# Performance work log

Measured on AMD Instinct MI355X. Metric: run time of the kernel, lower is better.

Reference implementation:

```python
import jax, jax.numpy as jnp
import numpy as np

# 4D convolution via lax.conv_general_dilated with 4 spatial dims.
# Layout: input (N, C, D, H, W, T), kernel (O, I, d, h, w, t).
DN = ('NCDHWT', 'OIDHWT', 'NCDHWT')


def conv4d(x, w, b, pad):
    # torch Conv2d/Conv4d is cross-correlation, matching lax.conv_general_dilated
    y = jax.lax.conv_general_dilated(
        x, w, window_strides=(1, 1, 1, 1),
        padding=[(pad, pad)] * 4, dimension_numbers=DN)
    return y + b.reshape(1, -1, 1, 1, 1, 1)


def _kaiming(key, shape):
    fan_out = shape[0] * int(np.prod(shape[2:]))
    std = np.sqrt(2.0 / fan_out)
    return (jax.random.normal(key, shape, dtype=jnp.float32) * std).astype(jnp.float32)


def setup_inputs() -> dict:
    key = jax.random.key(0)
    ks = jax.random.split(key, 11)
    B, W, H = 256, 16, 16
    corr = jax.random.normal(ks[0], (B, W * H, W, H), dtype=jnp.float32)
    w1 = _kaiming(ks[1], (1, 1, 17, 17, 9, 9))
    w2 = _kaiming(ks[2], (1, 1, 7, 7, 7, 7))
    w3 = _kaiming(ks[3], (1, 1, 5, 5, 5, 5))
    w4 = _kaiming(ks[4], (1, 1, 3, 3, 3, 3))
    w5 = _kaiming(ks[5], (1, 1, 8, 8, 1, 1))
    b1 = jax.random.normal(ks[6], (1,), dtype=jnp.float32) * 0.01
    b2 = jax.random.normal(ks[7], (1,), dtype=jnp.float32) * 0.01
    b3 = jax.random.normal(ks[8], (1,), dtype=jnp.float32) * 0.01
    b4 = jax.random.normal(ks[9], (1,), dtype=jnp.float32) * 0.01
    b5 = jax.random.normal(ks[10], (1,), dtype=jnp.float32) * 0.01
    return {"corr": corr, "w1": w1, "b1": b1, "w2": w2, "b2": b2,
            "w3": w3, "b3": b3, "w4": w4, "b4": b4, "w5": w5, "b5": b5}


def reference(corr, w1, b1, w2, b2, w3, b3, w4, b4, w5, b5):
    B, HW, W, H = corr.shape
    x = corr.reshape(B, 1, W, H, W, H)          # (B,1,16,16,16,16)
    x = jax.nn.relu(conv4d(x, w1, b1, 4))       # (B,1, 8, 8,16,16)
    x = jax.nn.relu(conv4d(x, w2, b2, 3))
    x = jax.nn.relu(conv4d(x, w3, b3, 2))
    x = jax.nn.relu(conv4d(x, w4, b4, 1))
    out = jax.nn.sigmoid(conv4d(x, w5, b5, 0))  # (B,1, 1, 1,16,16)
    return out.reshape(B, 1, W, H)
```

## Files before the change

kernel.cpp:

```cpp
#include <hip/hip_runtime.h>
#include <math.h>


typedef short bf16x8 __attribute__((ext_vector_type(8)));
typedef float f32x4 __attribute__((ext_vector_type(4)));
typedef unsigned int u32x4 __attribute__((ext_vector_type(4)));

#define XTS 64
#define NROWS 396
#define ZROW 384

__device__ __forceinline__ int xts(int row, int col) {
  return row * XTS + (col ^ ((row & 7) << 3));
}

__device__ __forceinline__ unsigned short f2bf(float f) {
  unsigned int u = __float_as_uint(f);
  u += 0x7fffu + ((u >> 16) & 1u);
  return (unsigned short)(u >> 16);
}

template <int KSZ, int PAD>
__device__ __forceinline__ void build_mid(const float* __restrict__ w,
                                          unsigned short* __restrict__ Bg, int gid) {
  const int lane = gid & 63;
  const int n_tile = (gid >> 6) & 3;
  const int chunk = (gid >> 8) & 1;
  const int tap = gid >> 9;
  const int kw = tap / KSZ, kt = tap - kw * KSZ;
  const int dh_o = n_tile * 16 + (lane & 15);
  const int d_o = dh_o >> 3, h_o = dh_o & 7;
  const int kbase = chunk * 32 + (lane >> 4) * 8;
  unsigned int pk[4];
#pragma unroll
  for (int p = 0; p < 4; ++p) {
    unsigned short half[2];
#pragma unroll
    for (int s = 0; s < 2; ++s) {
      const int k = kbase + p * 2 + s;
      const int d_i = k >> 3, h_i = k & 7;
      const int kd = d_i - d_o + PAD, kh = h_i - h_o + PAD;
      float v = 0.f;
      if (kd >= 0 && kd < KSZ && kh >= 0 && kh < KSZ)
        v = w[((kd * KSZ + kh) * KSZ + kw) * KSZ + kt];
      half[s] = f2bf(v);
    }
    pk[p] = (unsigned int)half[0] | ((unsigned int)half[1] << 16);
  }
  *(int4*)(Bg + (size_t)gid * 8) = make_int4(pk[0], pk[1], pk[2], pk[3]);
}

__global__ __launch_bounds__(256) void build_all(const float* __restrict__ w1,
                                                 const float* __restrict__ w2,
                                                 const float* __restrict__ w3,
                                                 const float* __restrict__ w4,
                                                 unsigned short* __restrict__ Bg1,
                                                 unsigned short* __restrict__ Bg2,
                                                 unsigned short* __restrict__ Bg3,
                                                 unsigned short* __restrict__ Bg4) {
  const int bid = blockIdx.x, tid = threadIdx.x;
  if (bid < 648) {
    const int gid = bid * 256 + tid;
    const int lane = gid & 63;
    const int n_tile = (gid >> 6) & 3;
    const int chunk = (gid >> 8) & 7;
    const int kwkt = gid >> 11;
    const int kw = kwkt / 9, kt = kwkt - kw * 9;
    const int dh_o = n_tile * 16 + (lane & 15);
    const int d_o = dh_o >> 3, h_o = dh_o & 7;
    const int kbase = chunk * 32 + (lane >> 4) * 8;
    unsigned int pk[4];
#pragma unroll
    for (int p = 0; p < 4; ++p) {
      unsigned short half[2];
#pragma unroll
      for (int s = 0; s < 2; ++s) {
        const int k = kbase + p * 2 + s;
        const int d_i = k >> 4, h_i = k & 15;
        const int kd = d_i - d_o + 4, kh = h_i - h_o + 4;
        float v = 0.f;
        if (kd >= 0 && kd < 17 && kh >= 0 && kh < 17)
          v = w1[((kd * 17 + kh) * 9 + kw) * 9 + kt];
        half[s] = f2bf(v);
      }
      pk[p] = (unsigned int)half[0] | ((unsigned int)half[1] << 16);
    }
    *(int4*)(Bg1 + (size_t)gid * 8) = make_int4(pk[0], pk[1], pk[2], pk[3]);
  } else if (bid < 746) {
    build_mid<7, 3>(w2, Bg2, (bid - 648) * 256 + tid);
  } else if (bid < 796) {
    build_mid<5, 2>(w3, Bg3, (bid - 746) * 256 + tid);
  } else {
    build_mid<3, 1>(w4, Bg4, (bid - 796) * 256 + tid);
  }
}

__device__ __forceinline__ void l1_load(const unsigned short* XT,
                                        const unsigned short* __restrict__ Bt,
                                        const int (&ar)[4], int kt, int col0, int col1,
                                        bf16x8 (&A)[8], bf16x8 (&B)[8]) {
#pragma unroll
  for (int m = 0; m < 4; ++m) {
    const int row = ar[m] + kt;
    const int sw = (row & 7) << 3;
    A[m] = *(const bf16x8*)&XT[row * XTS + (col0 ^ sw)];
    A[4 + m] = *(const bf16x8*)&XT[row * XTS + (col1 ^ sw)];
  }
#pragma unroll
  for (int c = 0; c < 2; ++c)
#pragma unroll
    for (int n = 0; n < 4; ++n)
      B[c * 4 + n] = *(const bf16x8*)(Bt + (size_t)kt * 16384 + c * 2048 + n * 512);
}

__device__ __forceinline__ void mfma16(const bf16x8 (&A)[8], const bf16x8 (&B)[8],
                                       f32x4 (&acc)[4][4]) {
#pragma unroll
  for (int c = 0; c < 2; ++c)
#pragma unroll
    for (int m = 0; m < 4; ++m)
#pragma unroll
      for (int n = 0; n < 4; ++n)
        acc[m][n] = __builtin_amdgcn_mfma_f32_16x16x32_bf16(A[c * 4 + m], B[c * 4 + n],
                                                            acc[m][n], 0, 0, 0);
}

__global__ __launch_bounds__(256) void conv_l1_mfma(const float* __restrict__ x,
                                                    const unsigned short* __restrict__ Bg,
                                                    float* __restrict__ P) {
  __shared__ __align__(16) unsigned short XT[NROWS * XTS];
  const int bx = blockIdx.x;
  const int b = bx >> 2, q = bx & 3;
  const int tid = threadIdx.x;
  const int lane = tid & 63, wave = tid >> 6;
  const int quad = lane >> 4, tl = lane & 15;
  const float* xb = x + (size_t)b * 65536;
  f32x4 acc[4][4] = {};

  for (int j = tid; j < (NROWS * XTS) / 8; j += 256)
    *(int4*)&XT[j * 8] = make_int4(0, 0, 0, 0);
  __syncthreads();

#pragma unroll
  for (int it = 0; it < 8; ++it) {
    const int i = tid + it * 256;
    const int dhp = i >> 6, wtq = i & 63;
    const int r0 = (wtq >> 2) * 24 + (wtq & 3) * 4 + 4;
    const float4 ra = *(const float4*)(xb + (size_t)(q * 64 + 2 * dhp) * 256 + wtq * 4);
    const float4 rb = *(const float4*)(xb + (size_t)(q * 64 + 2 * dhp + 1) * 256 + wtq * 4);
    const float a0[4] = {ra.x, ra.y, ra.z, ra.w};
    const float a1[4] = {rb.x, rb.y, rb.z, rb.w};
#pragma unroll
    for (int j = 0; j < 4; ++j) {
      const unsigned int p = (unsigned int)f2bf(a0[j]) | ((unsigned int)f2bf(a1[j]) << 16);
      *(unsigned int*)&XT[xts(r0 + j, dhp * 2)] = p;
    }
  }
  __syncthreads();

  const int chbase = q * 2;
  const unsigned short* Bt = Bg + (size_t)chbase * 2048 + lane * 8;
  const int col0 = quad * 8, col1 = col0 + 32;
  for (int kw = 0; kw < 9; ++kw) {
    int ar[4];
#pragma unroll
    for (int m = 0; m < 4; ++m) {
      const int w_i = wave * 4 + m + kw - 4;
      ar[m] = ((unsigned)w_i < 16u) ? (w_i * 24 + tl) : ZROW;
    }
    bf16x8 A0[8], B0[8], A1[8], B1[8];
    l1_load(XT, Bt, ar, 0, col0, col1, A0, B0);
#pragma unroll
    for (int kt = 0; kt < 9; ++kt) {
      if ((kt & 1) == 0) {
        if (kt < 8) l1_load(XT, Bt, ar, kt + 1, col0, col1, A1, B1);
        mfma16(A0, B0, acc);
      } else {
        if (kt < 8) l1_load(XT, Bt, ar, kt + 1, col0, col1, A0, B0);
        mfma16(A1, B1, acc);
      }
    }
    Bt += 9 * 16384;
  }

  float* Pb = P + (size_t)(q * 256 + b) * 16384;
#pragma unroll
  for (int m = 0; m < 4; ++m)
#pragma unroll
    for (int n = 0; n < 4; ++n) {
      const int dh_o = n * 16 + tl;
      const int wt0 = wave * 64 + m * 16 + quad * 4;
      *(float4*)&Pb[(size_t)dh_o * 256 + wt0] = *(const float4*)&acc[m][n];
    }
}

__device__ __forceinline__ void tl_load(const unsigned short* XT,
                                        const unsigned short* __restrict__ Bt,
                                        const int (&ar)[2], int kt, int nh, int col0,
                                        int col1, bf16x8 (&A)[4], bf16x8 (&B)[4]) {
#pragma unroll
  for (int m = 0; m < 2; ++m) {
    const int row = ar[m] + kt;
    const int sw = (row & 7) << 3;
    A[m] = *(const bf16x8*)&XT[row * XTS + (col0 ^ sw)];
    A[2 + m] = *(const bf16x8*)&XT[row * XTS + (col1 ^ sw)];
  }
#pragma unroll
  for (int c = 0; c < 2; ++c)
#pragma unroll
    for (int n = 0; n < 2; ++n)
      B[c * 2 + n] =
          *(const bf16x8*)(Bt + (size_t)kt * 4096 + c * 2048 + (nh * 2 + n) * 512);
}

__device__ __forceinline__ void mfma8(const bf16x8 (&A)[4], const bf16x8 (&B)[4],
                                      f32x4 (&acc)[2][2]) {
#pragma unroll
  for (int c = 0; c < 2; ++c)
#pragma unroll
    for (int m = 0; m < 2; ++m)
#pragma unroll
      for (int n = 0; n < 2; ++n)
        acc[m][n] = __builtin_amdgcn_mfma_f32_16x16x32_bf16(A[c * 2 + m], B[c * 2 + n],
                                                            acc[m][n], 0, 0, 0);
}

template <int KSZ, int PAD>
__device__ __forceinline__ void run_layer(unsigned short* XT,
                                          const unsigned short* __restrict__ Bg,
                                          const float bias, int mw, int nh, int lane,
                                          int quad, int tl) {
  f32x4 acc[2][2] = {};
  const unsigned short* Bt = Bg + lane * 8;
  const int col0 = quad * 8, col1 = col0 + 32;
  for (int kw = 0; kw < KSZ; ++kw) {
    int ar[2];
#pragma unroll
    for (int m = 0; m < 2; ++m) {
      const int w_i = mw * 2 + m + kw - PAD;
      ar[m] = ((unsigned)w_i < 16u) ? (w_i * 24 + tl + (4 - PAD)) : ZROW;
    }
    bf16x8 A0[4], B0[4], A1[4], B1[4];
    tl_load(XT, Bt, ar, 0, nh, col0, col1, A0, B0);
#pragma unroll
    for (int kt = 0; kt < KSZ; ++kt) {
      if ((kt & 1) == 0) {
        if (kt < KSZ - 1) tl_load(XT, Bt, ar, kt + 1, nh, col0, col1, A1, B1);
        mfma8(A0, B0, acc);
      } else {
        if (kt < KSZ - 1) tl_load(XT, Bt, ar, kt + 1, nh, col0, col1, A0, B0);
        mfma8(A1, B1, acc);
      }
    }
    Bt += (size_t)KSZ * 4096;
  }
  __syncthreads();
#pragma unroll
  for (int m = 0; m < 2; ++m) {
    const int rbase = (mw * 2 + m) * 24 + quad * 4 + 4;
#pragma unroll
    for (int n = 0; n < 2; ++n) {
      const int col = (nh * 2 + n) * 16 + tl;
#pragma unroll
      for (int j = 0; j < 4; ++j)
        XT[xts(rbase + j, col)] = f2bf(fmaxf(acc[m][n][j] + bias, 0.f));
    }
  }
  __syncthreads();
}

__global__ __launch_bounds__(1024) void tail_fused(const float* __restrict__ P,
                                                   const unsigned short* __restrict__ Bg2,
                                                   const unsigned short* __restrict__ Bg3,
                                                   const unsigned short* __restrict__ Bg4,
                                                   const float* __restrict__ b1,
                                                   const float* __restrict__ b2,
                                                   const float* __restrict__ b3,
                                                   const float* __restrict__ b4,
                                                   const float* __restrict__ w5,
                                                   const float* __restrict__ b5,
                                                   float* __restrict__ out) {
  __shared__ __align__(16) unsigned short XT[NROWS * XTS];
  const int b = blockIdx.x;
  const int tid = threadIdx.x;
  const int lane = tid & 63, wave = tid >> 6;
  const int quad = lane >> 4, tl = lane & 15;
  const int mw = wave >> 1, nh = wave & 1;
  const float* p0 = P + (size_t)b * 16384;
  const float* p1 = p0 + (size_t)256 * 16384;
  const float* p2 = p0 + (size_t)512 * 16384;
  const float* p3 = p0 + (size_t)768 * 16384;
  const float bias1 = b1[0];

  for (int j = tid; j < (NROWS * XTS) / 8; j += 1024)
    *(int4*)&XT[j * 8] = make_int4(0, 0, 0, 0);
  __syncthreads();

#pragma unroll
  for (int it = 0; it < 2; ++it) {
    const int i = tid + it * 1024;
    const int dhp = i >> 6, wtq = i & 63;
    const int r0 = (wtq >> 2) * 24 + (wtq & 3) * 4 + 4;
    const size_t off0 = (size_t)(2 * dhp) * 256 + wtq * 4;
    const float4 r0a = *(const float4*)(p0 + off0);
    const float4 r0b = *(const float4*)(p1 + off0);
    const float4 r0c = *(const float4*)(p2 + off0);
    const float4 r0d = *(const float4*)(p3 + off0);
    const float4 r1a = *(const float4*)(p0 + off0 + 256);
    const float4 r1b = *(const float4*)(p1 + off0 + 256);
    const float4 r1c = *(const float4*)(p2 + off0 + 256);
    const float4 r1d = *(const float4*)(p3 + off0 + 256);
    float a0[4] = {r0a.x + r0b.x + r0c.x + r0d.x, r0a.y + r0b.y + r0c.y + r0d.y,
                   r0a.z + r0b.z + r0c.z + r0d.z, r0a.w + r0b.w + r0c.w + r0d.w};
    float a1[4] = {r1a.x + r1b.x + r1c.x + r1d.x, r1a.y + r1b.y + r1c.y + r1d.y,
                   r1a.z + r1b.z + r1c.z + r1d.z, r1a.w + r1b.w + r1c.w + r1d.w};
#pragma unroll
    for (int j = 0; j < 4; ++j) {
      const unsigned short lo = f2bf(fmaxf(a0[j] + bias1, 0.f));
      const unsigned short hi = f2bf(fmaxf(a1[j] + bias1, 0.f));
      const unsigned int p = (unsigned int)lo | ((unsigned int)hi << 16);
      *(unsigned int*)&XT[xts(r0 + j, dhp * 2)] = p;
    }
  }
  __syncthreads();

  run_layer<7, 3>(XT, Bg2, b2[0], mw, nh, lane, quad, tl);
  run_layer<5, 2>(XT, Bg3, b3[0], mw, nh, lane, quad, tl);
  run_layer<3, 1>(XT, Bg4, b4[0], mw, nh, lane, quad, tl);

  if (tid < 256) {
    const int wt = tid;
    const int r = (wt >> 4) * 24 + (wt & 15) + 4;
    float s = b5[0];
#pragma unroll
    for (int k8 = 0; k8 < 8; ++k8) {
      const u32x4 v = *(const u32x4*)&XT[xts(r, k8 * 8)];
      const unsigned int uu[4] = {(unsigned int)v.x, (unsigned int)v.y, (unsigned int)v.z,
                                  (unsigned int)v.w};
#pragma unroll
      for (int p = 0; p < 4; ++p) {
        const float lo = __uint_as_float(uu[p] << 16);
        const float hi = __uint_as_float(uu[p] & 0xFFFF0000u);
        s += lo * w5[k8 * 8 + p * 2] + hi * w5[k8 * 8 + p * 2 + 1];
      }
    }
    out[(size_t)b * 256 + wt] = 1.f / (1.f + expf(-s));
  }
}

extern "C" void kernel_launch(void* const* d_in, const int* in_sizes, int n_in,
                              void* d_out, int out_size, void* d_ws, size_t ws_size,
                              hipStream_t stream) {
  const float* corr = (const float*)d_in[0];
  const float* w1 = (const float*)d_in[1];
  const float* b1 = (const float*)d_in[2];
  const float* w2 = (const float*)d_in[3];
  const float* b2 = (const float*)d_in[4];
  const float* w3 = (const float*)d_in[5];
  const float* b3 = (const float*)d_in[6];
  const float* w4 = (const float*)d_in[7];
  const float* b4 = (const float*)d_in[8];
  const float* w5 = (const float*)d_in[9];
  const float* b5 = (const float*)d_in[10];

  float* P = (float*)d_ws;
  unsigned short* Bg1 = (unsigned short*)((char*)d_ws + (64u << 20));
  unsigned short* Bg2 = Bg1 + (size_t)81 * 8 * 4 * 64 * 8;
  unsigned short* Bg3 = Bg2 + (size_t)49 * 2 * 4 * 64 * 8;
  unsigned short* Bg4 = Bg3 + (size_t)25 * 2 * 4 * 64 * 8;

  build_all<<<814, 256, 0, stream>>>(w1, w2, w3, w4, Bg1, Bg2, Bg3, Bg4);
  conv_l1_mfma<<<1024, 256, 0, stream>>>(corr, Bg1, P);
  tail_fused<<<256, 1024, 0, stream>>>(P, Bg2, Bg3, Bg4, b1, b2, b3, b4, w5, b5,
                                       (float*)d_out);
}
```

Before: 303.2 us.

## Restructure tail layers with padded LDS layout, larger per-wave tiles, fewer threads

The fused tail kernel now runs 512 threads instead of 1024, and each wave computes a 4x2 grid of MFMA tiles instead of 2x2, so each A fragment is reused across more outputs. The LDS activation buffer moves from an XOR-swizzled layout with halo rows to a padded-stride (72) layout with a single shared zero row. Out-of-range taps in both w and t are redirected to that zero row, which removes the full-buffer zeroing pass. The per-tap loop is flattened across kw/kt with double-buffered loads. The layer-1 MFMA loop also gets s_setprio raised around its MFMA bursts. The risks are fewer resident waves to hide LDS latency and higher register pressure from the larger accumulators.

```diff
diff --git a/kernel.cpp b/kernel.cpp
--- a/kernel.cpp
+++ b/kernel.cpp
@@ -9,6 +9,7 @@
 #define XTS 64
 #define NROWS 396
 #define ZROW 384
+#define TTS 72
 
 __device__ __forceinline__ int xts(int row, int col) {
   return row * XTS + (col ^ ((row & 7) << 3));
@@ -115,6 +116,7 @@
 
 __device__ __forceinline__ void mfma16(const bf16x8 (&A)[8], const bf16x8 (&B)[8],
                                        f32x4 (&acc)[4][4]) {
+  __builtin_amdgcn_s_setprio(1);
 #pragma unroll
   for (int c = 0; c < 2; ++c)
 #pragma unroll
@@ -123,6 +125,7 @@
       for (int n = 0; n < 4; ++n)
         acc[m][n] = __builtin_amdgcn_mfma_f32_16x16x32_bf16(A[c * 4 + m], B[c * 4 + n],
                                                             acc[m][n], 0, 0, 0);
+  __builtin_amdgcn_s_setprio(0);
 }
 
 __global__ __launch_bounds__(256) void conv_l1_mfma(const float* __restrict__ x,
@@ -194,93 +197,92 @@
     }
 }
 
-__device__ __forceinline__ void tl_load(const unsigned short* XT,
-                                        const unsigned short* __restrict__ Bt,
-                                        const int (&ar)[2], int kt, int nh, int col0,
-                                        int col1, bf16x8 (&A)[4], bf16x8 (&B)[4]) {
-#pragma unroll
-  for (int m = 0; m < 2; ++m) {
-    const int row = ar[m] + kt;
-    const int sw = (row & 7) << 3;
-    A[m] = *(const bf16x8*)&XT[row * XTS + (col0 ^ sw)];
-    A[2 + m] = *(const bf16x8*)&XT[row * XTS + (col1 ^ sw)];
-  }
+template <int KSZ, int PAD>
+__device__ __forceinline__ void tail_load_tap(const unsigned short* XT,
+                                              const unsigned short* __restrict__ Bg, int kwkt,
+                                              int mw, int nh, int lane, int quad, int tl,
+                                              bf16x8 (&A)[8], bf16x8 (&B)[4]) {
+  const int kw = kwkt / KSZ, kt = kwkt - kw * KSZ;
+  const int t_i = tl + kt - PAD;
+  const bool tv = (unsigned)t_i < 16u;
+  int ro[4];
+#pragma unroll
+  for (int m = 0; m < 4; ++m) {
+    const int w_i = mw * 4 + m + kw - PAD;
+    const bool v = tv && ((unsigned)w_i < 16u);
+    const int row = v ? (w_i * 16 + t_i) : 256;
+    ro[m] = row * TTS + quad * 8;
+  }
+#pragma unroll
+  for (int c = 0; c < 2; ++c)
+#pragma unroll
+    for (int m = 0; m < 4; ++m)
+      A[c * 4 + m] = *(const bf16x8*)&XT[ro[m] + c * 32];
 #pragma unroll
   for (int c = 0; c < 2; ++c)
 #pragma unroll
     for (int n = 0; n < 2; ++n)
       B[c * 2 + n] =
-          *(const bf16x8*)(Bt + (size_t)kt * 4096 + c * 2048 + (nh * 2 + n) * 512);
-}
-
-__device__ __forceinline__ void mfma8(const bf16x8 (&A)[4], const bf16x8 (&B)[4],
-                                      f32x4 (&acc)[2][2]) {
-#pragma unroll
-  for (int c = 0; c < 2; ++c)
-#pragma unroll
-    for (int m = 0; m < 2; ++m)
+          *(const bf16x8*)(Bg + (((size_t)(kwkt * 2 + c) * 4 + (nh * 2 + n)) << 9) + lane * 8);
+}
+
+__device__ __forceinline__ void mfma8(const bf16x8 (&A)[8], const bf16x8 (&B)[4],
+                                      f32x4 (&acc)[4][2]) {
+#pragma unroll
+  for (int c = 0; c < 2; ++c)
+#pragma unroll
+    for (int m = 0; m < 4; ++m)
 #pragma unroll
       for (int n = 0; n < 2; ++n)
-        acc[m][n] = __builtin_amdgcn_mfma_f32_16x16x32_bf16(A[c * 2 + m], B[c * 2 + n],
+        acc[m][n] = __builtin_amdgcn_mfma_f32_16x16x32_bf16(A[c * 4 + m], B[c * 2 + n],
                                                             acc[m][n], 0, 0, 0);
 }
 
-template <int KSZ, int PAD>
+template <int KSZ, int PAD, int NT>
 __device__ __forceinline__ void run_layer(unsigned short* XT,
                                           const unsigned short* __restrict__ Bg,
                                           const float bias, int mw, int nh, int lane,
                                           int quad, int tl) {
-  f32x4 acc[2][2] = {};
-  const unsigned short* Bt = Bg + lane * 8;
-  const int col0 = quad * 8, col1 = col0 + 32;
-  for (int kw = 0; kw < KSZ; ++kw) {
-    int ar[2];
-#pragma unroll
-    for (int m = 0; m < 2; ++m) {
-      const int w_i = mw * 2 + m + kw - PAD;
-      ar[m] = ((unsigned)w_i < 16u) ? (w_i * 24 + tl + (4 - PAD)) : ZROW;
-    }
-    bf16x8 A0[4], B0[4], A1[4], B1[4];
-    tl_load(XT, Bt, ar, 0, nh, col0, col1, A0, B0);
-#pragma unroll
-    for (int kt = 0; kt < KSZ; ++kt) {
-      if ((kt & 1) == 0) {
-        if (kt < KSZ - 1) tl_load(XT, Bt, ar, kt + 1, nh, col0, col1, A1, B1);
-        mfma8(A0, B0, acc);
-      } else {
-        if (kt < KSZ - 1) tl_load(XT, Bt, ar, kt + 1, nh, col0, col1, A0, B0);
-        mfma8(A1, B1, acc);
-      }
-    }
-    Bt += (size_t)KSZ * 4096;
-  }
-  __syncthreads();
-#pragma unroll
-  for (int m = 0; m < 2; ++m) {
-    const int rbase = (mw * 2 + m) * 24 + quad * 4 + 4;
+  f32x4 acc[4][2] = {};
+  {
+    bf16x8 A0[8], B0[4], A1[8], B1[4];
+    tail_load_tap<KSZ, PAD>(XT, Bg, 0, mw, nh, lane, quad, tl, A0, B0);
+    int k = 0;
+    while (true) {
+      if (k + 1 < NT) tail_load_tap<KSZ, PAD>(XT, Bg, k + 1, mw, nh, lane, quad, tl, A1, B1);
+      mfma8(A0, B0, acc);
+      if (++k >= NT) break;
+      if (k + 1 < NT) tail_load_tap<KSZ, PAD>(XT, Bg, k + 1, mw, nh, lane, quad, tl, A0, B0);
+      mfma8(A1, B1, acc);
+      if (++k >= NT) break;
+    }
+  }
+  __syncthreads();
+#pragma unroll
+  for (int m = 0; m < 4; ++m)
 #pragma unroll
     for (int n = 0; n < 2; ++n) {
       const int col = (nh * 2 + n) * 16 + tl;
+      const int wt0 = mw * 64 + m * 16 + quad * 4;
 #pragma unroll
       for (int j = 0; j < 4; ++j)
-        XT[xts(rbase + j, col)] = f2bf(fmaxf(acc[m][n][j] + bias, 0.f));
-    }
-  }
-  __syncthreads();
-}
-
-__global__ __launch_bounds__(1024) void tail_fused(const float* __restrict__ P,
-                                                   const unsigned short* __restrict__ Bg2,
-                                                   const unsigned short* __restrict__ Bg3,
-                                                   const unsigned short* __restrict__ Bg4,
-                                                   const float* __restrict__ b1,
-                                                   const float* __restrict__ b2,
-                                                   const float* __restrict__ b3,
-                                                   const float* __restrict__ b4,
-                                                   const float* __restrict__ w5,
-                                                   const float* __restrict__ b5,
-                                                   float* __restrict__ out) {
-  __shared__ __align__(16) unsigned short XT[NROWS * XTS];
+        XT[(wt0 + j) * TTS + col] = f2bf(fmaxf(acc[m][n][j] + bias, 0.f));
+    }
+  __syncthreads();
+}
+
+__global__ __launch_bounds__(512) void tail_fused(const float* __restrict__ P,
+                                                  const unsigned short* __restrict__ Bg2,
+                                                  const unsigned short* __restrict__ Bg3,
+                                                  const unsigned short* __restrict__ Bg4,
+                                                  const float* __restrict__ b1,
+                                                  const float* __restrict__ b2,
+                                                  const float* __restrict__ b3,
+                                                  const float* __restrict__ b4,
+                                                  const float* __restrict__ w5,
+                                                  const float* __restrict__ b5,
+                                                  float* __restrict__ out) {
+  __shared__ __align__(16) unsigned short XT[257 * TTS];
   const int b = blockIdx.x;
   const int tid = threadIdx.x;
   const int lane = tid & 63, wave = tid >> 6;
@@ -292,15 +294,11 @@
   const float* p3 = p0 + (size_t)768 * 16384;
   const float bias1 = b1[0];
 
-  for (int j = tid; j < (NROWS * XTS) / 8; j += 1024)
-    *(int4*)&XT[j * 8] = make_int4(0, 0, 0, 0);
-  __syncthreads();
-
-#pragma unroll
-  for (int it = 0; it < 2; ++it) {
-    const int i = tid + it * 1024;
+  if (tid < 9) *(int4*)&XT[256 * TTS + tid * 8] = make_int4(0, 0, 0, 0);
+#pragma unroll
+  for (int it = 0; it < 4; ++it) {
+    const int i = tid + it * 512;
     const int dhp = i >> 6, wtq = i & 63;
-    const int r0 = (wtq >> 2) * 24 + (wtq & 3) * 4 + 4;
     const size_t off0 = (size_t)(2 * dhp) * 256 + wtq * 4;
     const float4 r0a = *(const float4*)(p0 + off0);
     const float4 r0b = *(const float4*)(p1 + off0);
@@ -319,22 +317,22 @@
       const unsigned short lo = f2bf(fmaxf(a0[j] + bias1, 0.f));
       const unsigned short hi = f2bf(fmaxf(a1[j] + bias1, 0.f));
       const unsigned int p = (unsigned int)lo | ((unsigned int)hi << 16);
-      *(unsigned int*)&XT[xts(r0 + j, dhp * 2)] = p;
-    }
-  }
-  __syncthreads();
-
-  run_layer<7, 3>(XT, Bg2, b2[0], mw, nh, lane, quad, tl);
-  run_layer<5, 2>(XT, Bg3, b3[0], mw, nh, lane, quad, tl);
-  run_layer<3, 1>(XT, Bg4, b4[0], mw, nh, lane, quad, tl);
+      *(unsigned int*)&XT[(wtq * 4 + j) * TTS + dhp * 2] = p;
+    }
+  }
+  __syncthreads();
+
+  run_layer<7, 3, 49>(XT, Bg2, b2[0], mw, nh, lane, quad, tl);
+  run_layer<5, 2, 25>(XT, Bg3, b3[0], mw, nh, lane, quad, tl);
+  run_layer<3, 1, 9>(XT, Bg4, b4[0], mw, nh, lane, quad, tl);
 
   if (tid < 256) {
     const int wt = tid;
-    const int r = (wt >> 4) * 24 + (wt & 15) + 4;
     float s = b5[0];
+    const unsigned short* row = &XT[wt * TTS];
 #pragma unroll
     for (int k8 = 0; k8 < 8; ++k8) {
-      const u32x4 v = *(const u32x4*)&XT[xts(r, k8 * 8)];
+      const u32x4 v = *(const u32x4*)&row[k8 * 8];
       const unsigned int uu[4] = {(unsigned int)v.x, (unsigned int)v.y, (unsigned int)v.z,
                                   (unsigned int)v.w};
 #pragma unroll
@@ -371,6 +369,6 @@
 
   build_all<<<814, 256, 0, stream>>>(w1, w2, w3, w4, Bg1, Bg2, Bg3, Bg4);
   conv_l1_mfma<<<1024, 256, 0, stream>>>(corr, Bg1, P);
-  tail_fused<<<256, 1024, 0, stream>>>(P, Bg2, Bg3, Bg4, b1, b2, b3, b4, w5, b5,
-                                       (float*)d_out);
-}
+  tail_fused<<<256, 512, 0, stream>>>(P, Bg2, Bg3, Bg4, b1, b2, b3, b4, w5, b5,
+                                      (float*)d_out);
+}
```

Result: faster. 278.9 us (-8.0%).
